# Kernel optimization log

Measured on AMD Instinct MI355X. Metric: run time of the kernel, lower is better.

The kernel has to match this reference:

```python
import jax, jax.numpy as jnp
import numpy as np


def _mlp(x, ws, bs):
    # Linear->ReLU between layers, final Linear has no activation
    for i, (w, b) in enumerate(zip(ws, bs)):
        x = x @ w + b
        if i < len(ws) - 1:
            x = jax.nn.relu(x)
    return x


def setup_inputs() -> dict:
    key = jax.random.key(0)
    ks = jax.random.split(key, 24)
    n, q, H, W, dim = 2, 131072, 64, 2048, 64
    num = 4
    depth = jax.random.normal(ks[0], (n, 3, H, W), dtype=jnp.float32)
    feat = jax.random.normal(ks[1], (n, dim, H, W), dtype=jnp.float32)
    coord = jax.random.uniform(ks[2], (n, q, 2), dtype=jnp.float32, minval=-1.0, maxval=1.0)

    def lin(k, din, dout):
        kw, kb = jax.random.split(k)
        s = 1.0 / np.sqrt(din)
        w = jax.random.uniform(kw, (din, dout), minval=-s, maxval=s, dtype=jnp.float32)
        b = jax.random.uniform(kb, (dout,), minval=-s, maxval=s, dtype=jnp.float32)
        return w, b

    # pos_embedd: 2*num=8 -> [dim, num//2*dim] = [64,128] -> num*dim=256
    pe_dims = [2 * num, dim, (num // 2) * dim, num * dim]
    # encoder_xy: num*dim=256 -> [num*dim, num//2*dim, dim] = [256,128,64] -> num=4
    enc_dims = [num * dim, num * dim, (num // 2) * dim, dim, num]
    inp = {"depth": depth, "feat": feat, "coord": coord}
    for i in range(3):
        w, b = lin(ks[3 + i], pe_dims[i], pe_dims[i + 1])
        inp[f"pe_w{i}"] = w
        inp[f"pe_b{i}"] = b
    for i in range(4):
        w, b = lin(ks[8 + i], enc_dims[i], enc_dims[i + 1])
        inp[f"enc_w{i}"] = w
        inp[f"enc_b{i}"] = b
    return inp


def reference(depth, feat, coord,
              pe_w0, pe_b0, pe_w1, pe_b1, pe_w2, pe_b2,
              enc_w0, enc_b0, enc_w1, enc_b1, enc_w2, enc_b2, enc_w3, enc_b3):
    n, C, H, W = feat.shape
    q = coord.shape[1]
    eps = 1e-6
    # xy range-view magnitude map [n, H, W]
    xy = jnp.sqrt(depth[:, 1] ** 2 + depth[:, 2] ** 2)

    rx = 1.0 / H  # 2 / H / 2
    ry = 1.0 / W
    # offsets in the same (vx outer, vy inner) order as the torch loop
    offs = jnp.array([[-1.0, -1.0], [-1.0, 1.0], [1.0, -1.0], [1.0, 1.0]], dtype=coord.dtype)
    shift = offs * jnp.array([rx, ry], dtype=coord.dtype) + eps  # [4,2]
    c = jnp.clip(coord[None] + shift[:, None, None, :], -1.0 + 1e-6, 1.0 - 1e-6)  # [4,n,q,2]

    # nearest grid_sample, align_corners=False: unnormalized = ((g+1)*size - 1)/2, then round
    iy = jnp.clip(jnp.round(((c[..., 0] + 1.0) * H - 1.0) * 0.5).astype(jnp.int32), 0, H - 1)
    ix = jnp.clip(jnp.round(((c[..., 1] + 1.0) * W - 1.0) * 0.5).astype(jnp.int32), 0, W - 1)

    b = jnp.arange(n)[None, :, None]  # broadcasts against [4,n,q]
    q_feat = feat[b, :, iy, ix]      # [4,n,q,C] nearest-gathered features
    pred_xy = xy[b, iy, ix]          # [4,n,q]

    # sampled pixel-center coords (what grid_sample of feat_coord returns)
    qc_y = -1.0 + (2.0 * iy.astype(coord.dtype) + 1.0) / H
    qc_x = -1.0 + (2.0 * ix.astype(coord.dtype) + 1.0) / W
    rel = jnp.stack([(coord[None, ..., 0] - qc_y) * H,
                     (coord[None, ..., 1] - qc_x) * W], axis=-1)  # [4,n,q,2]

    # rearrange 't n q d -> (n q) (t d)'
    qf = q_feat.transpose(1, 2, 0, 3).reshape(n * q, 4 * C)
    rc = rel.transpose(1, 2, 0, 3).reshape(n * q, 4 * 2)

    qf = qf + _mlp(rc, [pe_w0, pe_w1, pe_w2], [pe_b0, pe_b1, pe_b2])
    logits = _mlp(qf, [enc_w0, enc_w1, enc_w2, enc_w3], [enc_b0, enc_b1, enc_b2, enc_b3])  # [nq,4]
    w = jax.nn.softmax(logits, axis=1)

    p = pred_xy.transpose(1, 2, 0).reshape(n * q, 4)  # 't n q -> (n q) t'
    ret = jnp.sum(p * w, axis=1).reshape(n, q, 1)     # [nq,1,4] @ [nq,4,1]
    return ret
```

## Files before the change

kernel.cpp:

```cpp
#include <hip/hip_runtime.h>
#include <hip/hip_runtime_api.h>
#include <math.h>

#define NBATCH 2
#define QQ     131072
#define HH     64
#define WWID   2048
#define CC     64
#define HWSZ   (HH*WWID)

constexpr int ROWS    = 32;
constexpr int THREADS = 256;

constexpr int ASTR_B = 512;

constexpr int OFF_A   = 0;
constexpr int OFF_TAP = 16384;
constexpr int OFF_PXY = OFF_TAP + 512;
constexpr int OFF_E3  = OFF_PXY + 512;
constexpr int LDS_BYTES = OFF_E3 + 1024;

constexpr int WOFF_PE0 = 0;
constexpr int WOFF_PE1 = 4096;
constexpr int WOFF_PE2 = 12288;
constexpr int WOFF_E0  = 45056;
constexpr int WOFF_E1  = 110592;
constexpr int WOFF_E2  = 143360;
constexpr int WTOTAL   = 151552;

typedef __attribute__((ext_vector_type(8))) short bf16x8;
typedef __attribute__((ext_vector_type(4))) float f32x4;

__device__ __forceinline__ ushort f2bf(float f) {
    union { float f; unsigned u; } x; x.f = f;
    unsigned r = x.u + 0x7fffu + ((x.u >> 16) & 1u);
    return (ushort)(r >> 16);
}
__device__ __forceinline__ float bf2f(ushort h) {
    union { unsigned u; float f; } x; x.u = ((unsigned)h) << 16;
    return x.f;
}
__device__ __forceinline__ unsigned cvtpk(float a, float b) {
    unsigned r;
    asm("v_cvt_pk_bf16_f32 %0, %1, %2" : "=v"(r) : "v"(a), "v"(b));
    return r;
}

__device__ __forceinline__ int swA(int row, int colByte) {
    return row * ASTR_B + (colByte ^ ((row & 7) << 4));
}

struct WDesc { const float* src; int K; int N; int kshift; };
struct WPack { WDesc d[6]; };

__global__ __launch_bounds__(256) void prep_weights(WPack p, ushort* __restrict__ dst)
{
    int e = blockIdx.x * 256 + threadIdx.x;
    int off = 0;
    #pragma unroll
    for (int L = 0; L < 6; ++L) {
        const int Kp = 1 << p.d[L].kshift;
        const int N  = p.d[L].N;
        const int sz = N * Kp;
        if (e < sz) {
            const int n = e / Kp;
            const int k = e & (Kp - 1);
            const float v = (k < p.d[L].K) ? p.d[L].src[(size_t)k * N + n] : 0.f;
            const int chunk = k >> 6;
            const int kk    = (k >> 5) & 1;
            const int tile  = chunk * ((N >> 4) * 2) + (n >> 4) * 2 + kk;
            const int lane  = (n & 15) + (((k >> 3) & 3) << 4);
            const int j     = k & 7;
            dst[off + tile * 512 + lane * 8 + j] = f2bf(v);
            return;
        }
        e -= sz; off += sz;
    }
}

__global__ __launch_bounds__(256) void prep_feat(
    const float* __restrict__ depth, const float* __restrict__ feat,
    ushort* __restrict__ nhwc, float* __restrict__ xy)
{
    const int idx = blockIdx.x * 256 + threadIdx.x;
    const int b   = idx >> 17;
    const int yx  = idx & (HWSZ - 1);

    const float d1 = depth[(b * 3 + 1) * HWSZ + yx];
    const float d2 = depth[(b * 3 + 2) * HWSZ + yx];
    xy[idx] = sqrtf(d1 * d1 + d2 * d2);

    const float* fp = feat + (size_t)b * CC * HWSZ + yx;
    ushort* op = nhwc + (size_t)idx * CC;
    #pragma unroll
    for (int c = 0; c < CC; c += 8) {
        union { uint4 v; ushort u[8]; } t;
        #pragma unroll
        for (int j = 0; j < 8; ++j) t.u[j] = f2bf(fp[(size_t)(c + j) * HWSZ]);
        *(uint4*)(op + c) = t.v;
    }
}

template <int K, int N, bool RELU>
__device__ __forceinline__ void dense_layer(
    char* __restrict__ sA, const ushort* __restrict__ Wt,
    const float* __restrict__ Bg, int tid)
{
    constexpr int TN  = N / 64;
    constexpr int NCH = K / 64;

    const int lane = tid & 63, wv = tid >> 6;
    const int wm = wv >> 2, wn = wv & 3;
    const int row0 = wm * 32;
    const int col0 = wn * (N / 4);
    const int lrow = lane & 15;
    const int lkb  = (lane >> 4) * 16;

    f32x4 acc[2][TN];
    #pragma unroll
    for (int tm = 0; tm < 2; ++tm)
        #pragma unroll
        for (int tn = 0; tn < TN; ++tn) acc[tm][tn] = (f32x4){0.f, 0.f, 0.f, 0.f};

    const char* wbase = (const char*)Wt + (size_t)lane * 16;

    for (int c = 0; c < NCH; ++c) {
        #pragma unroll
        for (int ks = 0; ks < 64; ks += 32) {
            const int cb = (c * 64 + ks) * 2 + lkb;
            const bf16x8 a0 = *(const bf16x8*)(sA + swA(row0 +      lrow, cb));
            const bf16x8 a1 = *(const bf16x8*)(sA + swA(row0 + 16 + lrow, cb));
            #pragma unroll
            for (int tn = 0; tn < TN; ++tn) {
                const int tile = c * ((N >> 4) * 2) + ((col0 >> 4) + tn) * 2 + (ks >> 5);
                const bf16x8 bw = *(const bf16x8*)(wbase + tile * 1024);
                acc[0][tn] = __builtin_amdgcn_mfma_f32_16x16x32_bf16(bw, a0, acc[0][tn], 0, 0, 0);
                acc[1][tn] = __builtin_amdgcn_mfma_f32_16x16x32_bf16(bw, a1, acc[1][tn], 0, 0, 0);
            }
        }
    }
    __syncthreads();

    #pragma unroll
    for (int tn = 0; tn < TN; ++tn) {
        const int colb = col0 + tn * 16 + (lane >> 4) * 4;
        const float4 b4 = *(const float4*)(Bg + colb);
        #pragma unroll
        for (int tm = 0; tm < 2; ++tm) {
            float v0 = acc[tm][tn][0] + b4.x;
            float v1 = acc[tm][tn][1] + b4.y;
            float v2 = acc[tm][tn][2] + b4.z;
            float v3 = acc[tm][tn][3] + b4.w;
            if (RELU) {
                v0 = fmaxf(v0, 0.f); v1 = fmaxf(v1, 0.f);
                v2 = fmaxf(v2, 0.f); v3 = fmaxf(v3, 0.f);
            }
            uint2 pk;
            pk.x = cvtpk(v0, v1);
            pk.y = cvtpk(v2, v3);
            const int row = row0 + tm * 16 + lrow;
            *(uint2*)(sA + swA(row, colb * 2)) = pk;
        }
    }
    __syncthreads();
}

template <bool USE_WS>
__global__ __launch_bounds__(256, 4) void fused_kernel(
    const float* __restrict__ depth, const float* __restrict__ feat,
    const float* __restrict__ coord,
    const float* __restrict__ pb0, const float* __restrict__ pb1,
    const float* __restrict__ pb2,
    const float* __restrict__ eb0, const float* __restrict__ eb1,
    const float* __restrict__ eb2,
    const float* __restrict__ ew3, const float* __restrict__ eb3,
    const ushort* __restrict__ wt,
    const ushort* __restrict__ nhwc, const float* __restrict__ xyws,
    float* __restrict__ out)
{
    extern __shared__ char lds[];
    char*  sA   = lds + OFF_A;
    int*   sTap = (int*)(lds + OFF_TAP);
    float* sPxy = (float*)(lds + OFF_PXY);
    float* sE3  = (float*)(lds + OFF_E3);

    const int tid  = threadIdx.x;
    const int row0g = blockIdx.x * ROWS;
    const int b     = row0g >> 17;

    sE3[tid] = ew3[tid];

    {
        const int r = tid >> 3, c16 = tid & 7;
        uint4 z; z.x = z.y = z.z = z.w = 0u;
        *(uint4*)(sA + r * ASTR_B + c16 * 16) = z;
    }
    __syncthreads();

    if (tid < 128) {
        #pragma clang fp contract(off)
        const int r = tid >> 2, s = tid & 3;
        const int row = row0g + r;
        const float cy = coord[row * 2 + 0];
        const float cx = coord[row * 2 + 1];
        const float offy = (s < 2) ? -1.f : 1.f;
        const float offx = (s & 1) ? 1.f : -1.f;
        const float rx = 1.f / (float)HH, ry = 1.f / (float)WWID;
        float ccy = cy + (offy * rx + 1e-6f);
        float ccx = cx + (offx * ry + 1e-6f);
        ccy = fminf(fmaxf(ccy, -1.f + 1e-6f), 1.f - 1e-6f);
        ccx = fminf(fmaxf(ccx, -1.f + 1e-6f), 1.f - 1e-6f);
        int iy = (int)rintf(((ccy + 1.f) * (float)HH - 1.f) * 0.5f);
        int ix = (int)rintf(((ccx + 1.f) * (float)WWID - 1.f) * 0.5f);
        iy = min(max(iy, 0), HH - 1);
        ix = min(max(ix, 0), WWID - 1);
        const float qcy = -1.f + (2.f * (float)iy + 1.f) / (float)HH;
        const float qcx = -1.f + (2.f * (float)ix + 1.f) / (float)WWID;
        *(ushort*)(sA + swA(r, s * 4 + 0)) = f2bf((cy - qcy) * (float)HH);
        *(ushort*)(sA + swA(r, s * 4 + 2)) = f2bf((cx - qcx) * (float)WWID);
        const int tap = iy * WWID + ix;
        sTap[r * 4 + s] = tap;
        float px;
        if (USE_WS) {
            px = xyws[b * HWSZ + tap];
        } else {
            const float d1 = depth[(b * 3 + 1) * HWSZ + tap];
            const float d2 = depth[(b * 3 + 2) * HWSZ + tap];
            px = sqrtf(d1 * d1 + d2 * d2);
        }
        sPxy[r * 4 + s] = px;
    }
    __syncthreads();

    dense_layer<64,  64,  true >(sA, wt + WOFF_PE0, pb0, tid);
    dense_layer<64,  128, true >(sA, wt + WOFF_PE1, pb1, tid);
    dense_layer<128, 256, false>(sA, wt + WOFF_PE2, pb2, tid);

    {
        const int gr = tid >> 3, h = tid & 7;
        const int gs = h >> 1, half = h & 1;
        const int tap = sTap[gr * 4 + gs];
        const int cb0 = gs * 128 + half * 64;
        if (USE_WS) {
            const ushort* src = nhwc + ((size_t)b * HWSZ + tap) * CC + half * 32;
            #pragma unroll
            for (int g = 0; g < 4; ++g) {
                char* dp = sA + swA(gr, cb0 + g * 16);
                union { uint4 v; ushort u[8]; } a, d;
                a.v = *(const uint4*)(src + g * 8);
                d.v = *(uint4*)dp;
                float s0 = bf2f(a.u[0]) + bf2f(d.u[0]);
                float s1 = bf2f(a.u[1]) + bf2f(d.u[1]);
                float s2 = bf2f(a.u[2]) + bf2f(d.u[2]);
                float s3 = bf2f(a.u[3]) + bf2f(d.u[3]);
                float s4 = bf2f(a.u[4]) + bf2f(d.u[4]);
                float s5 = bf2f(a.u[5]) + bf2f(d.u[5]);
                float s6 = bf2f(a.u[6]) + bf2f(d.u[6]);
                float s7 = bf2f(a.u[7]) + bf2f(d.u[7]);
                uint4 o;
                o.x = cvtpk(s0, s1); o.y = cvtpk(s2, s3);
                o.z = cvtpk(s4, s5); o.w = cvtpk(s6, s7);
                *(uint4*)dp = o;
            }
        } else {
            const float* fp = feat + (size_t)b * CC * HWSZ + tap;
            #pragma unroll 8
            for (int c = 0; c < 32; ++c) {
                const int ch = half * 32 + c;
                ushort* p = (ushort*)(sA + swA(gr, cb0 + c * 2));
                *p = f2bf(bf2f(*p) + fp[(size_t)ch * HWSZ]);
            }
        }
    }
    __syncthreads();

    dense_layer<256, 256, true>(sA, wt + WOFF_E0, eb0, tid);
    dense_layer<256, 128, true>(sA, wt + WOFF_E1, eb1, tid);
    dense_layer<128, 64,  true>(sA, wt + WOFF_E2, eb2, tid);

    if (tid < 128) {
        const int fr = tid >> 2, sub = tid & 3;
        float l0 = 0.f, l1 = 0.f, l2 = 0.f, l3 = 0.f;
        #pragma unroll
        for (int kk = 0; kk < 16; ++kk) {
            const int k = sub * 16 + kk;
            const float a = bf2f(*(const ushort*)(sA + swA(fr, k * 2)));
            const float4 w = ((const float4*)sE3)[k];
            l0 = fmaf(a, w.x, l0);
            l1 = fmaf(a, w.y, l1);
            l2 = fmaf(a, w.z, l2);
            l3 = fmaf(a, w.w, l3);
        }
        #pragma unroll
        for (int m = 1; m <= 2; m <<= 1) {
            l0 += __shfl_xor(l0, m);
            l1 += __shfl_xor(l1, m);
            l2 += __shfl_xor(l2, m);
            l3 += __shfl_xor(l3, m);
        }
        if (sub == 0) {
            l0 += eb3[0]; l1 += eb3[1]; l2 += eb3[2]; l3 += eb3[3];
            const float m  = fmaxf(fmaxf(l0, l1), fmaxf(l2, l3));
            const float e0 = expf(l0 - m), e1 = expf(l1 - m);
            const float e2 = expf(l2 - m), e3 = expf(l3 - m);
            const float inv = 1.f / (e0 + e1 + e2 + e3);
            const float o = (sPxy[fr * 4 + 0] * e0 + sPxy[fr * 4 + 1] * e1 +
                             sPxy[fr * 4 + 2] * e2 + sPxy[fr * 4 + 3] * e3) * inv;
            out[row0g + fr] = o;
        }
    }
}

extern "C" void kernel_launch(void* const* d_in, const int* in_sizes, int n_in,
                              void* d_out, int out_size, void* d_ws, size_t ws_size,
                              hipStream_t stream)
{
    const float* depth = (const float*)d_in[0];
    const float* feat  = (const float*)d_in[1];
    const float* coord = (const float*)d_in[2];
    const float* pw0 = (const float*)d_in[3],  *pb0 = (const float*)d_in[4];
    const float* pw1 = (const float*)d_in[5],  *pb1 = (const float*)d_in[6];
    const float* pw2 = (const float*)d_in[7],  *pb2 = (const float*)d_in[8];
    const float* ew0 = (const float*)d_in[9],  *eb0 = (const float*)d_in[10];
    const float* ew1 = (const float*)d_in[11], *eb1 = (const float*)d_in[12];
    const float* ew2 = (const float*)d_in[13], *eb2 = (const float*)d_in[14];
    const float* ew3 = (const float*)d_in[15], *eb3 = (const float*)d_in[16];
    float* out = (float*)d_out;

    const size_t nhwc_bytes = (size_t)NBATCH * HWSZ * CC * 2;
    const size_t xy_bytes   = (size_t)NBATCH * HWSZ * 4;
    const size_t wt_bytes   = (size_t)WTOTAL * 2;
    const bool use_ws = (ws_size >= nhwc_bytes + xy_bytes + wt_bytes);

    ushort* nhwc = (ushort*)d_ws;
    float*  xyws = (float*)((char*)d_ws + nhwc_bytes);
    ushort* wt   = use_ws ? (ushort*)((char*)d_ws + nhwc_bytes + xy_bytes)
                          : (ushort*)d_ws;

    WPack pack;
    pack.d[0] = { pw0, 8,   64,  6 };
    pack.d[1] = { pw1, 64,  128, 6 };
    pack.d[2] = { pw2, 128, 256, 7 };
    pack.d[3] = { ew0, 256, 256, 8 };
    pack.d[4] = { ew1, 256, 128, 8 };
    pack.d[5] = { ew2, 128, 64,  7 };
    prep_weights<<<WTOTAL / 256, 256, 0, stream>>>(pack, wt);

    const int nblocks = (NBATCH * QQ) / ROWS;

    if (use_ws) {
        prep_feat<<<(NBATCH * HWSZ) / 256, 256, 0, stream>>>(depth, feat, nhwc, xyws);
        fused_kernel<true><<<nblocks, THREADS, LDS_BYTES, stream>>>(
            depth, feat, coord, pb0, pb1, pb2, eb0, eb1, eb2, ew3, eb3,
            wt, nhwc, xyws, out);
    } else {
        fused_kernel<false><<<nblocks, THREADS, LDS_BYTES, stream>>>(
            depth, feat, coord, pb0, pb1, pb2, eb0, eb1, eb2, ew3, eb3,
            wt, nhwc, xyws, out);
    }
}
```

Measured before the change: 152.5 us.

## Double rows per block so each wave covers all 64 rows and reuses weight fragments

Each block now processes 64 query rows instead of 32. All four waves cover the full row range and split only the output columns, so each weight fragment loaded from global memory feeds four MFMAs instead of two. This halves per-row weight traffic and the block count, and the gather and softmax stages now use all threads. In exchange it doubles LDS use and accumulator registers, with launch bounds lowered to 3 blocks per CU, which may reduce occupancy and latency hiding for the gathers.

```diff
diff --git a/kernel.cpp b/kernel.cpp
--- a/kernel.cpp
+++ b/kernel.cpp
@@ -9,15 +9,15 @@
 #define CC     64
 #define HWSZ   (HH*WWID)
 
-constexpr int ROWS    = 32;
+constexpr int ROWS    = 64;
 constexpr int THREADS = 256;
 
 constexpr int ASTR_B = 512;
 
 constexpr int OFF_A   = 0;
-constexpr int OFF_TAP = 16384;
-constexpr int OFF_PXY = OFF_TAP + 512;
-constexpr int OFF_E3  = OFF_PXY + 512;
+constexpr int OFF_TAP = 32768;
+constexpr int OFF_PXY = OFF_TAP + 1024;
+constexpr int OFF_E3  = OFF_PXY + 1024;
 constexpr int LDS_BYTES = OFF_E3 + 1024;
 
 constexpr int WOFF_PE0 = 0;
@@ -110,15 +110,13 @@
     constexpr int NCH = K / 64;
 
     const int lane = tid & 63, wv = tid >> 6;
-    const int wm = wv >> 2, wn = wv & 3;
-    const int row0 = wm * 32;
-    const int col0 = wn * (N / 4);
+    const int col0 = wv * (N / 4);
     const int lrow = lane & 15;
     const int lkb  = (lane >> 4) * 16;
 
-    f32x4 acc[2][TN];
+    f32x4 acc[4][TN];
     #pragma unroll
-    for (int tm = 0; tm < 2; ++tm)
+    for (int tm = 0; tm < 4; ++tm)
         #pragma unroll
         for (int tn = 0; tn < TN; ++tn) acc[tm][tn] = (f32x4){0.f, 0.f, 0.f, 0.f};
 
@@ -128,14 +126,18 @@
         #pragma unroll
         for (int ks = 0; ks < 64; ks += 32) {
             const int cb = (c * 64 + ks) * 2 + lkb;
-            const bf16x8 a0 = *(const bf16x8*)(sA + swA(row0 +      lrow, cb));
-            const bf16x8 a1 = *(const bf16x8*)(sA + swA(row0 + 16 + lrow, cb));
+            const bf16x8 a0 = *(const bf16x8*)(sA + swA(     lrow, cb));
+            const bf16x8 a1 = *(const bf16x8*)(sA + swA(16 + lrow, cb));
+            const bf16x8 a2 = *(const bf16x8*)(sA + swA(32 + lrow, cb));
+            const bf16x8 a3 = *(const bf16x8*)(sA + swA(48 + lrow, cb));
             #pragma unroll
             for (int tn = 0; tn < TN; ++tn) {
                 const int tile = c * ((N >> 4) * 2) + ((col0 >> 4) + tn) * 2 + (ks >> 5);
                 const bf16x8 bw = *(const bf16x8*)(wbase + tile * 1024);
                 acc[0][tn] = __builtin_amdgcn_mfma_f32_16x16x32_bf16(bw, a0, acc[0][tn], 0, 0, 0);
                 acc[1][tn] = __builtin_amdgcn_mfma_f32_16x16x32_bf16(bw, a1, acc[1][tn], 0, 0, 0);
+                acc[2][tn] = __builtin_amdgcn_mfma_f32_16x16x32_bf16(bw, a2, acc[2][tn], 0, 0, 0);
+                acc[3][tn] = __builtin_amdgcn_mfma_f32_16x16x32_bf16(bw, a3, acc[3][tn], 0, 0, 0);
             }
         }
     }
@@ -146,7 +148,7 @@
         const int colb = col0 + tn * 16 + (lane >> 4) * 4;
         const float4 b4 = *(const float4*)(Bg + colb);
         #pragma unroll
-        for (int tm = 0; tm < 2; ++tm) {
+        for (int tm = 0; tm < 4; ++tm) {
             float v0 = acc[tm][tn][0] + b4.x;
             float v1 = acc[tm][tn][1] + b4.y;
             float v2 = acc[tm][tn][2] + b4.z;
@@ -158,7 +160,7 @@
             uint2 pk;
             pk.x = cvtpk(v0, v1);
             pk.y = cvtpk(v2, v3);
-            const int row = row0 + tm * 16 + lrow;
+            const int row = tm * 16 + lrow;
             *(uint2*)(sA + swA(row, colb * 2)) = pk;
         }
     }
@@ -166,7 +168,7 @@
 }
 
 template <bool USE_WS>
-__global__ __launch_bounds__(256, 4) void fused_kernel(
+__global__ __launch_bounds__(256, 3) void fused_kernel(
     const float* __restrict__ depth, const float* __restrict__ feat,
     const float* __restrict__ coord,
     const float* __restrict__ pb0, const float* __restrict__ pb1,
@@ -191,13 +193,14 @@
     sE3[tid] = ew3[tid];
 
     {
-        const int r = tid >> 3, c16 = tid & 7;
+        const int r = tid >> 2, q = tid & 3;
         uint4 z; z.x = z.y = z.z = z.w = 0u;
-        *(uint4*)(sA + r * ASTR_B + c16 * 16) = z;
-    }
-    __syncthreads();
-
-    if (tid < 128) {
+        *(uint4*)(sA + r * ASTR_B + q * 32)      = z;
+        *(uint4*)(sA + r * ASTR_B + q * 32 + 16) = z;
+    }
+    __syncthreads();
+
+    {
         #pragma clang fp contract(off)
         const int r = tid >> 2, s = tid & 3;
         const int row = row0g + r;
@@ -237,14 +240,13 @@
     dense_layer<128, 256, false>(sA, wt + WOFF_PE2, pb2, tid);
 
     {
-        const int gr = tid >> 3, h = tid & 7;
-        const int gs = h >> 1, half = h & 1;
+        const int gr = tid >> 2, gs = tid & 3;
         const int tap = sTap[gr * 4 + gs];
-        const int cb0 = gs * 128 + half * 64;
+        const int cb0 = gs * 128;
         if (USE_WS) {
-            const ushort* src = nhwc + ((size_t)b * HWSZ + tap) * CC + half * 32;
+            const ushort* src = nhwc + ((size_t)b * HWSZ + tap) * CC;
             #pragma unroll
-            for (int g = 0; g < 4; ++g) {
+            for (int g = 0; g < 8; ++g) {
                 char* dp = sA + swA(gr, cb0 + g * 16);
                 union { uint4 v; ushort u[8]; } a, d;
                 a.v = *(const uint4*)(src + g * 8);
@@ -265,10 +267,9 @@
         } else {
             const float* fp = feat + (size_t)b * CC * HWSZ + tap;
             #pragma unroll 8
-            for (int c = 0; c < 32; ++c) {
-                const int ch = half * 32 + c;
+            for (int c = 0; c < CC; ++c) {
                 ushort* p = (ushort*)(sA + swA(gr, cb0 + c * 2));
-                *p = f2bf(bf2f(*p) + fp[(size_t)ch * HWSZ]);
+                *p = f2bf(bf2f(*p) + fp[(size_t)c * HWSZ]);
             }
         }
     }
@@ -278,7 +279,7 @@
     dense_layer<256, 128, true>(sA, wt + WOFF_E1, eb1, tid);
     dense_layer<128, 64,  true>(sA, wt + WOFF_E2, eb2, tid);
 
-    if (tid < 128) {
+    {
         const int fr = tid >> 2, sub = tid & 3;
         float l0 = 0.f, l1 = 0.f, l2 = 0.f, l3 = 0.f;
         #pragma unroll
```

New measurement: 141.4 us. 1.08x faster.
